# Optimization experiments

Hardware: AMD Instinct MI355X
Metric: run time of the kernel (lower is better)

Reference implementation:

```python
import jax, jax.numpy as jnp
import numpy as np

B = 16384; NF = 16; VOCAB = 100000; ED = 32; NNUM = 13
E = 8; T = 2; H0 = 512; H1 = 256; TH = 128
D0 = NF * ED + NNUM  # 525
EPS = 1e-5


def setup_inputs() -> dict:
    key = jax.random.key(0)
    ks = jax.random.split(key, 24)
    f32 = jnp.float32
    return {
        "categorical_x": jax.random.randint(ks[0], (B, NF), 0, VOCAB),
        "numerical_x": jax.random.normal(ks[1], (B, NNUM), f32),
        "epoch": 5,  # >= M -> MoE (not if_neuron) branch
        "emb_table": jax.random.normal(ks[2], (NF * VOCAB, ED), f32) * 0.05,
        "W0": jax.random.normal(ks[3], (E, D0, H0), f32) * 0.05,
        "b0": jnp.zeros((E, H0), f32),
        "bn0_gamma": 1.0 + 0.1 * jax.random.normal(ks[4], (H0,), f32),
        "bn0_beta": 0.1 * jax.random.normal(ks[5], (H0,), f32),
        "bn0_mean": 0.1 * jax.random.normal(ks[6], (H0,), f32),
        "bn0_var": 0.5 + jax.random.uniform(ks[7], (H0,), f32),
        "W1": jax.random.normal(ks[8], (E, H0, H1), f32) * 0.05,
        "b1": jnp.zeros((E, H1), f32),
        "bn1_gamma": 1.0 + 0.1 * jax.random.normal(ks[9], (H1,), f32),
        "bn1_beta": 0.1 * jax.random.normal(ks[10], (H1,), f32),
        "bn1_mean": 0.1 * jax.random.normal(ks[11], (H1,), f32),
        "bn1_var": 0.5 + jax.random.uniform(ks[12], (H1,), f32),
        "Wg": jax.random.normal(ks[13], (T, D0, E), f32) * 0.05,
        "bg": jnp.zeros((T, E), f32),
        "Wt1": jax.random.normal(ks[14], (T, H1, TH), f32) * 0.05,
        "bt1": jnp.zeros((T, TH), f32),
        "tbn_gamma": 1.0 + 0.1 * jax.random.normal(ks[15], (T, TH), f32),
        "tbn_beta": 0.1 * jax.random.normal(ks[16], (T, TH), f32),
        "tbn_mean": 0.1 * jax.random.normal(ks[17], (T, TH), f32),
        "tbn_var": 0.5 + jax.random.uniform(ks[18], (T, TH), f32),
        "Wt2": jax.random.normal(ks[19], (T, TH, 1), f32) * 0.05,
        "bt2": jnp.zeros((T, 1), f32),
    }


def reference(categorical_x, numerical_x, epoch, emb_table,
              W0, b0, bn0_gamma, bn0_beta, bn0_mean, bn0_var,
              W1, b1, bn1_gamma, bn1_beta, bn1_mean, bn1_var,
              Wg, bg, Wt1, bt1, tbn_gamma, tbn_beta, tbn_mean, tbn_var,
              Wt2, bt2):
    # --- embedding + concat ---
    offsets = jnp.arange(NF, dtype=categorical_x.dtype) * VOCAB
    emb = emb_table[categorical_x + offsets[None, :]].reshape(B, NF * ED)
    x = jnp.concatenate([emb, numerical_x], axis=1)  # [B, D0]

    def bn(h, g, b, m, v):  # eval-mode BatchNorm1d, params shared across experts
        return (h - m) * jax.lax.rsqrt(v + EPS) * g + b

    # --- per-expert layer 0: grouped GEMM + shared BN/ReLU (Dropout eval=id) ---
    h = jnp.einsum('bd,edk->ebk', x, W0) + b0[:, None, :]          # [E,B,H0]
    h = jax.nn.relu(bn(h, bn0_gamma, bn0_beta, bn0_mean, bn0_var))
    # --- per-expert layer 1 ---
    h = jnp.einsum('ebd,edk->ebk', h, W1) + b1[:, None, :]          # [E,B,H1]
    h = jax.nn.relu(bn(h, bn1_gamma, bn1_beta, bn1_mean, bn1_var))

    expert_output = jnp.transpose(h, (1, 0, 2))                     # [B,E,H1]
    # --- per-task softmax gates over the raw input, bmm combine ---
    gates = jax.nn.softmax(jnp.einsum('bd,tde->tbe', x, Wg) + bg[:, None, :], axis=-1)  # [T,B,E]
    fea = jnp.einsum('tbe,bek->tbk', gates, expert_output)          # [T,B,H1]

    # --- per-task tower MLP: Linear -> BN -> ReLU -> Linear, sigmoid ---
    t = jnp.einsum('tbk,tkh->tbh', fea, Wt1) + bt1[:, None, :]      # [T,B,TH]
    t = (t - tbn_mean[:, None, :]) * jax.lax.rsqrt(tbn_var[:, None, :] + EPS)
    t = jax.nn.relu(t * tbn_gamma[:, None, :] + tbn_beta[:, None, :])
    out = (jnp.einsum('tbh,tho->tbo', t, Wt2) + bt2[:, None, :])[..., 0]  # [T,B]
    return jax.nn.sigmoid(out)
```

## Files before the change

### kernel.cpp

```cpp
#include <hip/hip_runtime.h>
#include <hip/hip_bf16.h>

#define B_ 16384
#define NF_ 16
#define VOCAB_ 100000
#define ED_ 32
#define NNUM_ 13
#define E_ 8
#define T_ 2
#define H0_ 512
#define H1_ 256
#define TH_ 128
#define D0_ 525
#define K0P 576

#define BM 128
#define BN 128
#define BKK 64

typedef __bf16 bf16x8 __attribute__((ext_vector_type(8)));
typedef float  f32x4  __attribute__((ext_vector_type(4)));
typedef int    i32x4  __attribute__((ext_vector_type(4)));

__global__ __launch_bounds__(192) void k_embed(const int* __restrict__ cat,
                                               const float* __restrict__ num,
                                               const float* __restrict__ emb,
                                               __hip_bfloat16* __restrict__ x) {
  int b = blockIdx.x;
  int t = threadIdx.x;
  const int* crow = cat + b * NF_;
#pragma unroll
  for (int i = 0; i < 3; ++i) {
    int d = t + i * 192;
    float v;
    if (d < 512) {
      int f = d >> 5, c = d & 31;
      v = emb[((long long)(f * VOCAB_ + crow[f])) * ED_ + c];
    } else if (d < D0_) {
      v = num[b * NNUM_ + (d - 512)];
    } else {
      v = 0.f;
    }
    x[(long long)b * K0P + d] = __float2bfloat16(v);
  }
}

__global__ __launch_bounds__(256) void k_wprep(const float* __restrict__ W,
                                               __hip_bfloat16* __restrict__ Wp,
                                               int K, int N, int KP) {
  __shared__ float tile[64][65];
  int k0 = blockIdx.x * 64, n0 = blockIdx.y * 64, e = blockIdx.z;
  int tx = threadIdx.x & 63, ty = threadIdx.x >> 6;
  for (int r = ty; r < 64; r += 4) {
    int k = k0 + r;
    tile[r][tx] = (k < K) ? W[((long long)e * K + k) * N + n0 + tx] : 0.f;
  }
  __syncthreads();
  for (int r = ty; r < 64; r += 4) {
    int n = n0 + r;
    Wp[((long long)e * N + n) * KP + k0 + tx] = __float2bfloat16(tile[tx][r]);
  }
}

__global__ void k_prep_small(const float* b0, const float* g0, const float* be0,
                             const float* m0, const float* v0,
                             const float* b1, const float* g1, const float* be1,
                             const float* m1, const float* v1,
                             const float* bt1, const float* tg, const float* tb,
                             const float* tm, const float* tv,
                             float* scale0, float* ebias0, float* scale1, float* ebias1,
                             float* tscale, float* tbias) {
  int i = blockIdx.x * 256 + threadIdx.x;
  if (i < H0_) scale0[i] = g0[i] * rsqrtf(v0[i] + 1e-5f);
  if (i < H1_) scale1[i] = g1[i] * rsqrtf(v1[i] + 1e-5f);
  if (i < T_ * TH_) {
    float s = tg[i] * rsqrtf(tv[i] + 1e-5f);
    tscale[i] = s;
    tbias[i] = (bt1[i] - tm[i]) * s + tb[i];
  }
  if (i < E_ * H0_) {
    int n = i & (H0_ - 1);
    float s = g0[n] * rsqrtf(v0[n] + 1e-5f);
    ebias0[i] = (b0[i] - m0[n]) * s + be0[n];
  }
  if (i < E_ * H1_) {
    int n = i & (H1_ - 1);
    float s = g1[n] * rsqrtf(v1[n] + 1e-5f);
    ebias1[i] = (b1[i] - m1[n]) * s + be1[n];
  }
}

__global__ __launch_bounds__(256) void k_gates(const __hip_bfloat16* __restrict__ x,
                                               const float* __restrict__ Wg,
                                               const float* __restrict__ bg,
                                               float* __restrict__ gates) {
  int gidx = blockIdx.x * 256 + threadIdx.x;
  int b = gidx >> 4, te = gidx & 15;
  int t = te >> 3, e = te & 7;
  const __hip_bfloat16* xr = x + (long long)b * K0P;
  const float* wg = Wg + ((long long)t * D0_) * E_ + e;
  float acc = bg[t * E_ + e];
  int k = 0;
  for (; k + 8 <= D0_; k += 8) {
    bf16x8 xv = *reinterpret_cast<const bf16x8*>(xr + k);
#pragma unroll
    for (int j = 0; j < 8; ++j)
      acc += (float)xv[j] * wg[(long long)(k + j) * E_];
  }
  for (; k < D0_; ++k) acc += __bfloat162float(xr[k]) * wg[(long long)k * E_];
  float mx = acc;
#pragma unroll
  for (int o = 1; o < 8; o <<= 1) mx = fmaxf(mx, __shfl_xor(mx, o));
  float p = __expf(acc - mx);
  float s = p;
#pragma unroll
  for (int o = 1; o < 8; o <<= 1) s += __shfl_xor(s, o);
  gates[((long long)t * B_ + b) * E_ + e] = p / s;
}

__global__ __launch_bounds__(256) void k_gemm(
    const __hip_bfloat16* __restrict__ Aall, long long strideAe, int lda,
    const __hip_bfloat16* __restrict__ Ball, long long strideBe, int ldb,
    __hip_bfloat16* __restrict__ Call, long long strideCe, int N,
    const float* __restrict__ scale, const float* __restrict__ ebias, int strideEb,
    int K) {
  __shared__ __align__(16) char As[BM * 128];
  __shared__ __align__(16) char Bs[BN * 128];

  const int e = blockIdx.z;
  const char* A = reinterpret_cast<const char*>(Aall + (long long)e * strideAe +
                                                (long long)blockIdx.x * BM * lda);
  const char* Bw = reinterpret_cast<const char*>(Ball + (long long)e * strideBe +
                                                 (long long)blockIdx.y * BN * ldb);
  const int ldab = lda * 2, ldbb = ldb * 2;

  const int tid = threadIdx.x;
  const int lane = tid & 63;
  const int wid = tid >> 6;
  const int wr = wid >> 1, wc = wid & 1;
  const int srow = tid >> 3;
  const int sc16 = (tid & 7) * 16;

  i32x4 ra[4], rb[4];
  const int nk = K / BKK;

#pragma unroll
  for (int it = 0; it < 4; ++it) {
    int row = srow + it * 32;
    ra[it] = *reinterpret_cast<const i32x4*>(A + (long long)row * ldab + sc16);
    rb[it] = *reinterpret_cast<const i32x4*>(Bw + (long long)row * ldbb + sc16);
  }

  f32x4 acc[4][4];
#pragma unroll
  for (int m = 0; m < 4; ++m)
#pragma unroll
    for (int n = 0; n < 4; ++n) acc[m][n] = (f32x4){0.f, 0.f, 0.f, 0.f};

  for (int ks = 0; ks < nk; ++ks) {
    __syncthreads();
#pragma unroll
    for (int it = 0; it < 4; ++it) {
      int row = srow + it * 32;
      int byt = row * 128 + (sc16 ^ ((row & 7) << 4));
      *reinterpret_cast<i32x4*>(As + byt) = ra[it];
      *reinterpret_cast<i32x4*>(Bs + byt) = rb[it];
    }
    if (ks + 1 < nk) {
#pragma unroll
      for (int it = 0; it < 4; ++it) {
        int row = srow + it * 32;
        ra[it] = *reinterpret_cast<const i32x4*>(A + (long long)row * ldab + (ks + 1) * 128 + sc16);
        rb[it] = *reinterpret_cast<const i32x4*>(Bw + (long long)row * ldbb + (ks + 1) * 128 + sc16);
      }
    }
    __syncthreads();
#pragma unroll
    for (int kk = 0; kk < 2; ++kk) {
      bf16x8 af[4], bfr[4];
      int kb = kk * 64 + (lane >> 4) * 16;
#pragma unroll
      for (int m = 0; m < 4; ++m) {
        int row = wr * 64 + m * 16 + (lane & 15);
        af[m] = *reinterpret_cast<const bf16x8*>(As + row * 128 + (kb ^ ((row & 7) << 4)));
      }
#pragma unroll
      for (int n = 0; n < 4; ++n) {
        int row = wc * 64 + n * 16 + (lane & 15);
        bfr[n] = *reinterpret_cast<const bf16x8*>(Bs + row * 128 + (kb ^ ((row & 7) << 4)));
      }
#pragma unroll
      for (int m = 0; m < 4; ++m)
#pragma unroll
        for (int n = 0; n < 4; ++n)
          acc[m][n] = __builtin_amdgcn_mfma_f32_16x16x32_bf16(af[m], bfr[n], acc[m][n], 0, 0, 0);
    }
  }

  __hip_bfloat16* C = Call + (long long)e * strideCe;
  const float* eb = ebias + e * strideEb;
  const int m0 = blockIdx.x * BM, n0 = blockIdx.y * BN;
#pragma unroll
  for (int n = 0; n < 4; ++n) {
    int col = n0 + wc * 64 + n * 16 + (lane & 15);
    float s = scale[col];
    float bb = eb[col];
#pragma unroll
    for (int m = 0; m < 4; ++m) {
      int rowb = m0 + wr * 64 + m * 16 + (lane >> 4) * 4;
#pragma unroll
      for (int i = 0; i < 4; ++i) {
        float v = fmaxf(acc[m][n][i] * s + bb, 0.f);
        C[(long long)(rowb + i) * N + col] = __float2bfloat16(v);
      }
    }
  }
}

__global__ __launch_bounds__(256) void k_tower(
    const __hip_bfloat16* __restrict__ h1, const float* __restrict__ gates,
    const float* __restrict__ Wt1, const float* __restrict__ Wt2,
    const float* __restrict__ bt2, const float* __restrict__ tscale,
    const float* __restrict__ tbias, float* __restrict__ out) {
  __shared__ __align__(16) char Ws[TH_ * 512];
  const int t = blockIdx.y;
  const int tid = threadIdx.x;
  const int lane = tid & 63, wv = tid >> 6;

  for (int it = 0; it < 16; ++it) {
    int idx = it * 256 + tid;
    int h = idx & 127, kc = idx >> 7;
    bf16x8 v;
#pragma unroll
    for (int j = 0; j < 8; ++j)
      v[j] = (__bf16)Wt1[((long long)t * H1_ + kc * 8 + j) * TH_ + h];
    int byt = h * 512 + ((kc * 16) ^ ((h & 7) << 4));
    *reinterpret_cast<bf16x8*>(Ws + byt) = v;
  }

  const int row = blockIdx.x * 64 + wv * 16 + (lane & 15);
  const int g4 = lane >> 4;

  float gt[8];
  {
    const float* gp = gates + ((long long)t * B_ + row) * E_;
#pragma unroll
    for (int j = 0; j < 8; ++j) gt[j] = gp[j];
  }

  float fa[8][8];
#pragma unroll
  for (int c = 0; c < 8; ++c)
#pragma unroll
    for (int j = 0; j < 8; ++j) fa[c][j] = 0.f;

#pragma unroll
  for (int ee = 0; ee < 8; ++ee) {
    const char* hp = reinterpret_cast<const char*>(h1) +
                     (((long long)ee * B_ + row) * H1_ + g4 * 8) * 2;
    float g = gt[ee];
#pragma unroll
    for (int c = 0; c < 8; ++c) {
      bf16x8 hv = *reinterpret_cast<const bf16x8*>(hp + c * 64);
#pragma unroll
      for (int j = 0; j < 8; ++j) fa[c][j] += g * (float)hv[j];
    }
  }
  bf16x8 af[8];
#pragma unroll
  for (int c = 0; c < 8; ++c)
#pragma unroll
    for (int j = 0; j < 8; ++j) af[c][j] = (__bf16)fa[c][j];

  __syncthreads();

  f32x4 acc[8];
#pragma unroll
  for (int n = 0; n < 8; ++n) acc[n] = (f32x4){0.f, 0.f, 0.f, 0.f};
#pragma unroll
  for (int c = 0; c < 8; ++c) {
    int kb = c * 64 + g4 * 16;
#pragma unroll
    for (int n = 0; n < 8; ++n) {
      int hrow = n * 16 + (lane & 15);
      bf16x8 bv = *reinterpret_cast<const bf16x8*>(Ws + hrow * 512 + (kb ^ ((hrow & 7) << 4)));
      acc[n] = __builtin_amdgcn_mfma_f32_16x16x32_bf16(af[c], bv, acc[n], 0, 0, 0);
    }
  }

  float part[4] = {0.f, 0.f, 0.f, 0.f};
#pragma unroll
  for (int n = 0; n < 8; ++n) {
    int col = n * 16 + (lane & 15);
    float s = tscale[t * TH_ + col], bb = tbias[t * TH_ + col], w2 = Wt2[t * TH_ + col];
#pragma unroll
    for (int i = 0; i < 4; ++i)
      part[i] += fmaxf(acc[n][i] * s + bb, 0.f) * w2;
  }
#pragma unroll
  for (int o = 1; o < 16; o <<= 1) {
#pragma unroll
    for (int i = 0; i < 4; ++i) part[i] += __shfl_xor(part[i], o);
  }
  if ((lane & 15) == 0) {
    int rbase = blockIdx.x * 64 + wv * 16 + g4 * 4;
    float b2 = bt2[t];
#pragma unroll
    for (int i = 0; i < 4; ++i) {
      float z = part[i] + b2;
      out[(long long)t * B_ + rbase + i] = 1.f / (1.f + __expf(-z));
    }
  }
}

extern "C" void kernel_launch(void* const* d_in, const int* in_sizes, int n_in,
                              void* d_out, int out_size, void* d_ws, size_t ws_size,
                              hipStream_t stream) {
  const int*   cat = (const int*)d_in[0];
  const float* num = (const float*)d_in[1];
  const float* emb = (const float*)d_in[3];
  const float* W0  = (const float*)d_in[4];
  const float* b0  = (const float*)d_in[5];
  const float* g0  = (const float*)d_in[6];
  const float* be0 = (const float*)d_in[7];
  const float* m0  = (const float*)d_in[8];
  const float* v0  = (const float*)d_in[9];
  const float* W1  = (const float*)d_in[10];
  const float* b1  = (const float*)d_in[11];
  const float* g1  = (const float*)d_in[12];
  const float* be1 = (const float*)d_in[13];
  const float* m1  = (const float*)d_in[14];
  const float* v1  = (const float*)d_in[15];
  const float* Wg  = (const float*)d_in[16];
  const float* bg  = (const float*)d_in[17];
  const float* Wt1 = (const float*)d_in[18];
  const float* bt1 = (const float*)d_in[19];
  const float* tg  = (const float*)d_in[20];
  const float* tb  = (const float*)d_in[21];
  const float* tm  = (const float*)d_in[22];
  const float* tv  = (const float*)d_in[23];
  const float* Wt2 = (const float*)d_in[24];
  const float* bt2 = (const float*)d_in[25];
  float* out = (float*)d_out;

  char* ws = (char*)d_ws;
  if (ws_size < 228094976ULL) return;

  __hip_bfloat16* x_bf = (__hip_bfloat16*)(ws + 0ULL);
  __hip_bfloat16* W0p  = (__hip_bfloat16*)(ws + 18874368ULL);
  __hip_bfloat16* W1p  = (__hip_bfloat16*)(ws + 23592960ULL);
  float* gates   = (float*)(ws + 25690112ULL);
  float* scale0  = (float*)(ws + 26738688ULL);
  float* ebias0  = (float*)(ws + 26740736ULL);
  float* scale1  = (float*)(ws + 26757120ULL);
  float* ebias1  = (float*)(ws + 26758144ULL);
  float* tscale  = (float*)(ws + 26766336ULL);
  float* tbias   = (float*)(ws + 26767360ULL);
  __hip_bfloat16* h0 = (__hip_bfloat16*)(ws + 26768384ULL);
  __hip_bfloat16* h1 = (__hip_bfloat16*)(ws + 160986112ULL);

  k_wprep<<<dim3(K0P / 64, H0_ / 64, E_), 256, 0, stream>>>(W0, W0p, D0_, H0_, K0P);
  k_wprep<<<dim3(H0_ / 64, H1_ / 64, E_), 256, 0, stream>>>(W1, W1p, H0_, H1_, H0_);
  k_prep_small<<<16, 256, 0, stream>>>(b0, g0, be0, m0, v0, b1, g1, be1, m1, v1,
                                       bt1, tg, tb, tm, tv,
                                       scale0, ebias0, scale1, ebias1, tscale, tbias);
  k_embed<<<B_, 192, 0, stream>>>(cat, num, emb, x_bf);
  k_gates<<<B_ * 16 / 256, 256, 0, stream>>>(x_bf, Wg, bg, gates);
  k_gemm<<<dim3(B_ / BM, H0_ / BN, E_), 256, 0, stream>>>(
      x_bf, 0LL, K0P, W0p, (long long)H0_ * K0P, K0P,
      h0, (long long)B_ * H0_, H0_, scale0, ebias0, H0_, K0P);
  k_gemm<<<dim3(B_ / BM, H1_ / BN, E_), 256, 0, stream>>>(
      h0, (long long)B_ * H0_, H0_, W1p, (long long)H1_ * H0_, H0_,
      h1, (long long)B_ * H1_, H1_, scale1, ebias1, H1_, H0_);
  k_tower<<<dim3(B_ / 64, T_), 256, 0, stream>>>(h1, gates, Wt1, Wt2, bt2,
                                                 tscale, tbias, out);
}
```

Baseline: 253.6 us.

## Use direct global-to-LDS loads in GEMM and merge both tasks in tower kernel

The grouped GEMM now stages A and B tiles with global_load_lds (direct global-to-LDS copies) and a pre-swizzled address instead of register prefetch plus ds_write, adding a trailing barrier each k-step. This removes the register round-trip but also drops the software prefetch overlap. The tower kernel now handles both tasks in one block, so the expert outputs h1 are read once and combined with both gate sets, halving h1 traffic at the cost of more registers and two Wt1 LDS fills per block.

```diff
diff --git a/kernel.cpp b/kernel.cpp
--- a/kernel.cpp
+++ b/kernel.cpp
@@ -21,6 +21,13 @@
 typedef __bf16 bf16x8 __attribute__((ext_vector_type(8)));
 typedef float  f32x4  __attribute__((ext_vector_type(4)));
 typedef int    i32x4  __attribute__((ext_vector_type(4)));
+
+typedef __attribute__((address_space(3))) void lds_void;
+typedef __attribute__((address_space(1))) const void gbl_void;
+
+__device__ __forceinline__ void load_lds16(const void* g, void* l) {
+  __builtin_amdgcn_global_load_lds((gbl_void*)g, (lds_void*)l, 16, 0, 0);
+}
 
 __global__ __launch_bounds__(192) void k_embed(const int* __restrict__ cat,
                                                const float* __restrict__ num,
@@ -138,41 +145,24 @@
   const int lane = tid & 63;
   const int wid = tid >> 6;
   const int wr = wid >> 1, wc = wid & 1;
-  const int srow = tid >> 3;
-  const int sc16 = (tid & 7) * 16;
-
-  i32x4 ra[4], rb[4];
+
+  const int baserow = wid * 32 + (lane >> 3);
+  const int swz = ((lane & 7) << 4) ^ ((lane >> 3) << 4);
+
+  f32x4 acc[4][4];
+#pragma unroll
+  for (int m = 0; m < 4; ++m)
+#pragma unroll
+    for (int n = 0; n < 4; ++n) acc[m][n] = (f32x4){0.f, 0.f, 0.f, 0.f};
+
   const int nk = K / BKK;
-
-#pragma unroll
-  for (int it = 0; it < 4; ++it) {
-    int row = srow + it * 32;
-    ra[it] = *reinterpret_cast<const i32x4*>(A + (long long)row * ldab + sc16);
-    rb[it] = *reinterpret_cast<const i32x4*>(Bw + (long long)row * ldbb + sc16);
-  }
-
-  f32x4 acc[4][4];
-#pragma unroll
-  for (int m = 0; m < 4; ++m)
-#pragma unroll
-    for (int n = 0; n < 4; ++n) acc[m][n] = (f32x4){0.f, 0.f, 0.f, 0.f};
-
   for (int ks = 0; ks < nk; ++ks) {
-    __syncthreads();
-#pragma unroll
-    for (int it = 0; it < 4; ++it) {
-      int row = srow + it * 32;
-      int byt = row * 128 + (sc16 ^ ((row & 7) << 4));
-      *reinterpret_cast<i32x4*>(As + byt) = ra[it];
-      *reinterpret_cast<i32x4*>(Bs + byt) = rb[it];
-    }
-    if (ks + 1 < nk) {
-#pragma unroll
-      for (int it = 0; it < 4; ++it) {
-        int row = srow + it * 32;
-        ra[it] = *reinterpret_cast<const i32x4*>(A + (long long)row * ldab + (ks + 1) * 128 + sc16);
-        rb[it] = *reinterpret_cast<const i32x4*>(Bw + (long long)row * ldbb + (ks + 1) * 128 + sc16);
-      }
+    const int kb0 = ks * 128;
+#pragma unroll
+    for (int i = 0; i < 4; ++i) {
+      const int row = baserow + i * 8;
+      load_lds16(A + (long long)row * ldab + kb0 + swz, As + (wid * 4 + i) * 1024);
+      load_lds16(Bw + (long long)row * ldbb + kb0 + swz, Bs + (wid * 4 + i) * 1024);
     }
     __syncthreads();
 #pragma unroll
@@ -195,6 +185,7 @@
         for (int n = 0; n < 4; ++n)
           acc[m][n] = __builtin_amdgcn_mfma_f32_16x16x32_bf16(af[m], bfr[n], acc[m][n], 0, 0, 0);
     }
+    __syncthreads();
   }
 
   __hip_bfloat16* C = Call + (long long)e * strideCe;
@@ -223,92 +214,102 @@
     const float* __restrict__ bt2, const float* __restrict__ tscale,
     const float* __restrict__ tbias, float* __restrict__ out) {
   __shared__ __align__(16) char Ws[TH_ * 512];
-  const int t = blockIdx.y;
   const int tid = threadIdx.x;
   const int lane = tid & 63, wv = tid >> 6;
 
-  for (int it = 0; it < 16; ++it) {
-    int idx = it * 256 + tid;
-    int h = idx & 127, kc = idx >> 7;
-    bf16x8 v;
-#pragma unroll
-    for (int j = 0; j < 8; ++j)
-      v[j] = (__bf16)Wt1[((long long)t * H1_ + kc * 8 + j) * TH_ + h];
-    int byt = h * 512 + ((kc * 16) ^ ((h & 7) << 4));
-    *reinterpret_cast<bf16x8*>(Ws + byt) = v;
-  }
-
   const int row = blockIdx.x * 64 + wv * 16 + (lane & 15);
   const int g4 = lane >> 4;
 
-  float gt[8];
+  float gt0[8], gt1[8];
   {
-    const float* gp = gates + ((long long)t * B_ + row) * E_;
-#pragma unroll
-    for (int j = 0; j < 8; ++j) gt[j] = gp[j];
-  }
-
-  float fa[8][8];
+    const float* gp0 = gates + (long long)row * E_;
+    const float* gp1 = gates + ((long long)B_ + row) * E_;
+#pragma unroll
+    for (int j = 0; j < 8; ++j) { gt0[j] = gp0[j]; gt1[j] = gp1[j]; }
+  }
+
+  float fa0[8][8], fa1[8][8];
 #pragma unroll
   for (int c = 0; c < 8; ++c)
 #pragma unroll
-    for (int j = 0; j < 8; ++j) fa[c][j] = 0.f;
+    for (int j = 0; j < 8; ++j) { fa0[c][j] = 0.f; fa1[c][j] = 0.f; }
 
 #pragma unroll
   for (int ee = 0; ee < 8; ++ee) {
     const char* hp = reinterpret_cast<const char*>(h1) +
                      (((long long)ee * B_ + row) * H1_ + g4 * 8) * 2;
-    float g = gt[ee];
+    float ga = gt0[ee], gb = gt1[ee];
 #pragma unroll
     for (int c = 0; c < 8; ++c) {
       bf16x8 hv = *reinterpret_cast<const bf16x8*>(hp + c * 64);
 #pragma unroll
-      for (int j = 0; j < 8; ++j) fa[c][j] += g * (float)hv[j];
-    }
-  }
-  bf16x8 af[8];
+      for (int j = 0; j < 8; ++j) {
+        float v = (float)hv[j];
+        fa0[c][j] += ga * v;
+        fa1[c][j] += gb * v;
+      }
+    }
+  }
+  bf16x8 af0[8], af1[8];
 #pragma unroll
   for (int c = 0; c < 8; ++c)
 #pragma unroll
-    for (int j = 0; j < 8; ++j) af[c][j] = (__bf16)fa[c][j];
-
-  __syncthreads();
-
-  f32x4 acc[8];
-#pragma unroll
-  for (int n = 0; n < 8; ++n) acc[n] = (f32x4){0.f, 0.f, 0.f, 0.f};
-#pragma unroll
-  for (int c = 0; c < 8; ++c) {
-    int kb = c * 64 + g4 * 16;
+    for (int j = 0; j < 8; ++j) {
+      af0[c][j] = (__bf16)fa0[c][j];
+      af1[c][j] = (__bf16)fa1[c][j];
+    }
+
+#pragma unroll
+  for (int t = 0; t < T_; ++t) {
+    if (t) __syncthreads();
+    for (int it = 0; it < 16; ++it) {
+      int idx = it * 256 + tid;
+      int h = idx & 127, kc = idx >> 7;
+      bf16x8 v;
+#pragma unroll
+      for (int j = 0; j < 8; ++j)
+        v[j] = (__bf16)Wt1[((long long)t * H1_ + kc * 8 + j) * TH_ + h];
+      int byt = h * 512 + ((kc * 16) ^ ((h & 7) << 4));
+      *reinterpret_cast<bf16x8*>(Ws + byt) = v;
+    }
+    __syncthreads();
+
+    f32x4 acc[8];
+#pragma unroll
+    for (int n = 0; n < 8; ++n) acc[n] = (f32x4){0.f, 0.f, 0.f, 0.f};
+#pragma unroll
+    for (int c = 0; c < 8; ++c) {
+      int kb = c * 64 + g4 * 16;
+#pragma unroll
+      for (int n = 0; n < 8; ++n) {
+        int hrow = n * 16 + (lane & 15);
+        bf16x8 bv = *reinterpret_cast<const bf16x8*>(Ws + hrow * 512 + (kb ^ ((hrow & 7) << 4)));
+        acc[n] = __builtin_amdgcn_mfma_f32_16x16x32_bf16(t ? af1[c] : af0[c], bv, acc[n], 0, 0, 0);
+      }
+    }
+
+    float part[4] = {0.f, 0.f, 0.f, 0.f};
 #pragma unroll
     for (int n = 0; n < 8; ++n) {
-      int hrow = n * 16 + (lane & 15);
-      bf16x8 bv = *reinterpret_cast<const bf16x8*>(Ws + hrow * 512 + (kb ^ ((hrow & 7) << 4)));
-      acc[n] = __builtin_amdgcn_mfma_f32_16x16x32_bf16(af[c], bv, acc[n], 0, 0, 0);
-    }
-  }
-
-  float part[4] = {0.f, 0.f, 0.f, 0.f};
-#pragma unroll
-  for (int n = 0; n < 8; ++n) {
-    int col = n * 16 + (lane & 15);
-    float s = tscale[t * TH_ + col], bb = tbias[t * TH_ + col], w2 = Wt2[t * TH_ + col];
-#pragma unroll
-    for (int i = 0; i < 4; ++i)
-      part[i] += fmaxf(acc[n][i] * s + bb, 0.f) * w2;
-  }
-#pragma unroll
-  for (int o = 1; o < 16; o <<= 1) {
-#pragma unroll
-    for (int i = 0; i < 4; ++i) part[i] += __shfl_xor(part[i], o);
-  }
-  if ((lane & 15) == 0) {
-    int rbase = blockIdx.x * 64 + wv * 16 + g4 * 4;
-    float b2 = bt2[t];
-#pragma unroll
-    for (int i = 0; i < 4; ++i) {
-      float z = part[i] + b2;
-      out[(long long)t * B_ + rbase + i] = 1.f / (1.f + __expf(-z));
+      int col = n * 16 + (lane & 15);
+      float s = tscale[t * TH_ + col], bb = tbias[t * TH_ + col], w2 = Wt2[t * TH_ + col];
+#pragma unroll
+      for (int i = 0; i < 4; ++i)
+        part[i] += fmaxf(acc[n][i] * s + bb, 0.f) * w2;
+    }
+#pragma unroll
+    for (int o = 1; o < 16; o <<= 1) {
+#pragma unroll
+      for (int i = 0; i < 4; ++i) part[i] += __shfl_xor(part[i], o);
+    }
+    if ((lane & 15) == 0) {
+      int rbase = blockIdx.x * 64 + wv * 16 + g4 * 4;
+      float b2 = bt2[t];
+#pragma unroll
+      for (int i = 0; i < 4; ++i) {
+        float z = part[i] + b2;
+        out[(long long)t * B_ + rbase + i] = 1.f / (1.f + __expf(-z));
+      }
     }
   }
 }
@@ -372,6 +373,6 @@
   k_gemm<<<dim3(B_ / BM, H1_ / BN, E_), 256, 0, stream>>>(
       h0, (long long)B_ * H0_, H0_, W1p, (long long)H1_ * H0_, H0_,
       h1, (long long)B_ * H1_, H1_, scale1, ebias1, H1_, H0_);
-  k_tower<<<dim3(B_ / 64, T_), 256, 0, stream>>>(h1, gates, Wt1, Wt2, bt2,
-                                                 tscale, tbias, out);
-}
+  k_tower<<<dim3(B_ / 64), 256, 0, stream>>>(h1, gates, Wt1, Wt2, bt2,
+                                             tscale, tbias, out);
+}
```

Result: slower. 312.9 us (+23.4%).
